# Kernel optimization log

Measured on AMD Instinct MI355X. Metric: run time of the kernel, lower is better.

## Reference

```python
import jax, jax.numpy as jnp
import numpy as np

N = 50000
E = 800000
D = 128
NCLASS = 10


def setup_inputs() -> dict:
    key = jax.random.key(0)
    ks = jax.random.split(key, 12)
    stdv = 1.0 / np.sqrt(D)
    inp = {
        "x": jax.random.normal(ks[0], (N, D), dtype=jnp.float32),
        "edge_src": jax.random.randint(ks[1], (E,), 0, N, dtype=jnp.int32),
        "edge_dst": jax.random.randint(ks[2], (E,), 0, N, dtype=jnp.int32),
        "edge_weight": jax.random.uniform(ks[3], (E,), dtype=jnp.float32),
        "W1": jax.random.uniform(ks[4], (D, D), jnp.float32, -stdv, stdv),
        "b1": jax.random.uniform(ks[5], (D,), jnp.float32, -stdv, stdv),
        "W2": jax.random.uniform(ks[6], (D, D), jnp.float32, -stdv, stdv),
        "b2": jax.random.uniform(ks[7], (D,), jnp.float32, -stdv, stdv),
        "W3": jax.random.uniform(ks[8], (D, D), jnp.float32, -stdv, stdv),
        "b3": jax.random.uniform(ks[9], (D,), jnp.float32, -stdv, stdv),
        "lin_W": jax.random.normal(ks[10], (NCLASS, 3 * D), dtype=jnp.float32) * 0.05,
        "lin_b": jax.random.normal(ks[11], (NCLASS,), dtype=jnp.float32) * 0.05,
    }
    return inp


def _gcn_layer(h, W, b, edge_src, edge_dst, edge_weight):
    # support = h @ W  (dense GEMM), then spmm(adj, support) as gather-scale-scatter
    support = h @ W                                   # [N, out]
    msgs = support[edge_src] * edge_weight[:, None]   # [E, out]
    agg = jax.ops.segment_sum(msgs, edge_dst, num_segments=h.shape[0])
    return agg + b


def reference(x, edge_src, edge_dst, edge_weight, W1, b1, W2, b2, W3, b3, lin_W, lin_b):
    x1 = jax.nn.relu(_gcn_layer(x, W1, b1, edge_src, edge_dst, edge_weight))
    o1 = jnp.max(x1, axis=0)
    x2 = jax.nn.relu(_gcn_layer(x1, W2, b2, edge_src, edge_dst, edge_weight))
    o2 = jnp.max(x2, axis=0)
    x3 = _gcn_layer(x2, W3, b3, edge_src, edge_dst, edge_weight)
    o3 = jnp.max(x3, axis=0)
    lin_in = jnp.concatenate([o1, o2, o3], axis=0)    # [3*D]
    logits = lin_W @ lin_in + lin_b                   # [nclass]
    return jax.nn.log_softmax(logits, axis=0)
```

## Files before the change

kernel.cpp:

```cpp
#include <hip/hip_runtime.h>
#include <hip/hip_bf16.h>
#include <math.h>

#define NN 50000
#define NPAD 50048
#define NE 800000
#define DD 128
#define NCLS 10
#define SCAN_BLOCK 1024
#define NTILES ((NN + 1 + SCAN_BLOCK - 1) / SCAN_BLOCK)

typedef short s16x8 __attribute__((ext_vector_type(8)));
typedef float f32x4 __attribute__((ext_vector_type(4)));

__device__ __forceinline__ unsigned short f2bf(float x) {
  __hip_bfloat16 h = __float2bfloat16(x);
  return __builtin_bit_cast(unsigned short, h);
}
__device__ __forceinline__ float bflo(unsigned int u) { return __uint_as_float(u << 16); }
__device__ __forceinline__ float bfhi(unsigned int u) { return __uint_as_float(u & 0xFFFF0000u); }

__device__ __forceinline__ unsigned int fkey(float f) {
  unsigned int u = __float_as_uint(f);
  return u ^ ((u & 0x80000000u) ? 0xFFFFFFFFu : 0x80000000u);
}
__device__ __forceinline__ float funkey(unsigned int k) {
  unsigned int u = (k & 0x80000000u) ? (k ^ 0x80000000u) : ~k;
  return __uint_as_float(u);
}

__global__ void k_init(int* __restrict__ offs, unsigned int* __restrict__ omax) {
  int i = blockIdx.x * blockDim.x + threadIdx.x;
  if (i < NN + 1) offs[i] = 0;
  if (i < 3 * DD) omax[i] = 0u;
}

__global__ void k_count(const int* __restrict__ edst, int* __restrict__ offs) {
  int e = blockIdx.x * blockDim.x + threadIdx.x;
  if (e < NE) atomicAdd(&offs[edst[e] + 1], 1);
}

__global__ void k_scan_partial(const int* __restrict__ offs, int* __restrict__ bsum) {
  __shared__ int red[SCAN_BLOCK];
  int i = blockIdx.x * SCAN_BLOCK + threadIdx.x;
  red[threadIdx.x] = (i < NN + 1) ? offs[i] : 0;
  __syncthreads();
  for (int off = SCAN_BLOCK / 2; off > 0; off >>= 1) {
    if ((int)threadIdx.x < off) red[threadIdx.x] += red[threadIdx.x + off];
    __syncthreads();
  }
  if (threadIdx.x == 0) bsum[blockIdx.x] = red[0];
}

__global__ void k_scan_bsum(int* __restrict__ bsum) {
  if (threadIdx.x == 0) {
    int run = 0;
    for (int i = 0; i < NTILES; ++i) { int v = bsum[i]; bsum[i] = run; run += v; }
  }
}

__global__ void k_scan_final(int* __restrict__ offs, const int* __restrict__ bsum,
                             int* __restrict__ cursor) {
  __shared__ int tmp[SCAN_BLOCK];
  int i = blockIdx.x * SCAN_BLOCK + threadIdx.x;
  int v = (i < NN + 1) ? offs[i] : 0;
  tmp[threadIdx.x] = v;
  __syncthreads();
  for (int off = 1; off < SCAN_BLOCK; off <<= 1) {
    int t = ((int)threadIdx.x >= off) ? tmp[threadIdx.x - off] : 0;
    __syncthreads();
    tmp[threadIdx.x] += t;
    __syncthreads();
  }
  int incl = tmp[threadIdx.x] + bsum[blockIdx.x];
  if (i < NN + 1) {
    offs[i] = incl;
    if (i < NN) cursor[i] = incl;
  }
}

__global__ void k_fill(const int* __restrict__ esrc, const int* __restrict__ edst,
                       const float* __restrict__ ew, int* __restrict__ cursor,
                       int2* __restrict__ csr) {
  int e = blockIdx.x * blockDim.x + threadIdx.x;
  if (e < NE) {
    int d = edst[e];
    int p = atomicAdd(&cursor[d], 1);
    csr[p] = make_int2(esrc[e], __float_as_int(ew[e]));
  }
}

__global__ __launch_bounds__(256) void k_cvtW(const float* __restrict__ W1,
    const float* __restrict__ W2, const float* __restrict__ W3,
    unsigned short* __restrict__ WT1, unsigned short* __restrict__ WT2,
    unsigned short* __restrict__ WT3) {
  int i = blockIdx.x * 256 + threadIdx.x;
  if (i < DD * DD) {
    int k = i >> 7, c = i & 127;
    WT1[c * DD + k] = f2bf(W1[i]);
    WT2[c * DD + k] = f2bf(W2[i]);
    WT3[c * DD + k] = f2bf(W3[i]);
  }
}

template <int F32IN>
__global__ __launch_bounds__(256) void k_mm(const void* __restrict__ Hv,
                                            const unsigned short* __restrict__ Wt,
                                            unsigned short* __restrict__ S) {
  __shared__ unsigned short Hl[32 * DD];
  char* lb = (char*)Hl;
  const int wave = threadIdx.x >> 6, lane = threadIdx.x & 63;
  const int l15 = lane & 15, lk16 = (lane >> 4);
  const int r0 = blockIdx.x * 32;

#pragma unroll
  for (int j = 0; j < 2; ++j) {
    const int idx = threadIdx.x + j * 256;
    const int B = idx * 16;
    const int row = B >> 8;
    const int addr = B ^ ((row & 7) << 4);
    if (F32IN) {
      const float* H = (const float*)Hv;
      const int r = r0 + row;
      float4 a = make_float4(0.f, 0.f, 0.f, 0.f), b = a;
      if (r < NN) {
        const float* src = H + (size_t)r * DD + ((B & 255) >> 1);
        a = *(const float4*)src;
        b = *(const float4*)(src + 4);
      }
      uint4 pv;
      pv.x = (uint)f2bf(a.x) | ((uint)f2bf(a.y) << 16);
      pv.y = (uint)f2bf(a.z) | ((uint)f2bf(a.w) << 16);
      pv.z = (uint)f2bf(b.x) | ((uint)f2bf(b.y) << 16);
      pv.w = (uint)f2bf(b.z) | ((uint)f2bf(b.w) << 16);
      *(uint4*)(lb + addr) = pv;
    } else {
      const char* H = (const char*)Hv;
      uint4 v = *(const uint4*)(H + (size_t)r0 * 256 + B);
      *(uint4*)(lb + addr) = v;
    }
  }
  __syncthreads();

  const int cbase = wave * 32;
  s16x8 Af[2][4];
#pragma unroll
  for (int m = 0; m < 2; ++m)
#pragma unroll
    for (int ks = 0; ks < 4; ++ks)
      Af[m][ks] = *(const s16x8*)&Wt[(cbase + m * 16 + l15) * DD + ks * 32 + lk16 * 8];

  s16x8 Bf[2][4];
#pragma unroll
  for (int n = 0; n < 2; ++n) {
    const int row = n * 16 + l15;
#pragma unroll
    for (int ks = 0; ks < 4; ++ks) {
      const int B = row * 256 + ks * 64 + lk16 * 16;
      Bf[n][ks] = *(const s16x8*)(lb + (B ^ ((row & 7) << 4)));
    }
  }

  f32x4 acc[2][2];
#pragma unroll
  for (int m = 0; m < 2; ++m)
#pragma unroll
    for (int n = 0; n < 2; ++n) acc[m][n] = (f32x4){0.f, 0.f, 0.f, 0.f};

#pragma unroll
  for (int ks = 0; ks < 4; ++ks)
#pragma unroll
    for (int m = 0; m < 2; ++m)
#pragma unroll
      for (int n = 0; n < 2; ++n)
        acc[m][n] = __builtin_amdgcn_mfma_f32_16x16x32_bf16(Af[m][ks], Bf[n][ks],
                                                            acc[m][n], 0, 0, 0);

  __syncthreads();
#pragma unroll
  for (int m = 0; m < 2; ++m)
#pragma unroll
    for (int n = 0; n < 2; ++n) {
      const int row = n * 16 + l15;
      const int colb = (cbase + m * 16 + 4 * lk16) * 2;
      const int B = row * 256 + colb;
      uint2 pv;
      pv.x = (uint)f2bf(acc[m][n][0]) | ((uint)f2bf(acc[m][n][1]) << 16);
      pv.y = (uint)f2bf(acc[m][n][2]) | ((uint)f2bf(acc[m][n][3]) << 16);
      *(uint2*)(lb + (B ^ ((row & 7) << 4))) = pv;
    }
  __syncthreads();
#pragma unroll
  for (int j = 0; j < 2; ++j) {
    const int idx = threadIdx.x + j * 256;
    const int B = idx * 16;
    const int row = B >> 8;
    uint4 v = *(const uint4*)(lb + (B ^ ((row & 7) << 4)));
    *(uint4*)((char*)S + (size_t)r0 * 256 + B) = v;
  }
}

__device__ __forceinline__ void fma8(float* acc, float w, uint4 u) {
  acc[0] = fmaf(w, bflo(u.x), acc[0]);
  acc[1] = fmaf(w, bfhi(u.x), acc[1]);
  acc[2] = fmaf(w, bflo(u.y), acc[2]);
  acc[3] = fmaf(w, bfhi(u.y), acc[3]);
  acc[4] = fmaf(w, bflo(u.z), acc[4]);
  acc[5] = fmaf(w, bfhi(u.z), acc[5]);
  acc[6] = fmaf(w, bflo(u.w), acc[6]);
  acc[7] = fmaf(w, bfhi(u.w), acc[7]);
}

__global__ __launch_bounds__(256) void k_agg(const unsigned short* __restrict__ S,
                                             const int2* __restrict__ csr,
                                             const int* __restrict__ offs,
                                             const float* __restrict__ bias,
                                             unsigned short* __restrict__ Xout,
                                             unsigned int* __restrict__ omax,
                                             int do_relu) {
  __shared__ unsigned int cmax[DD];
  for (int i = threadIdx.x; i < DD; i += 256) cmax[i] = 0u;
  __syncthreads();
  const int lane = threadIdx.x & 63;
  const int wave = threadIdx.x >> 6;
  const int q = lane >> 4;
  const int t = lane & 15;
  const int gwave = blockIdx.x * 4 + wave;
  const int nwaves = gridDim.x * 4;
  const unsigned short* Scol = S + t * 8;

  float bcol[8];
  {
    float4 b0 = *(const float4*)&bias[t * 8];
    float4 b1 = *(const float4*)&bias[t * 8 + 4];
    bcol[0] = b0.x; bcol[1] = b0.y; bcol[2] = b0.z; bcol[3] = b0.w;
    bcol[4] = b1.x; bcol[5] = b1.y; bcol[6] = b1.z; bcol[7] = b1.w;
  }
  float mx[8];
#pragma unroll
  for (int j = 0; j < 8; ++j) mx[j] = -INFINITY;

  for (int d = gwave; d < NN; d += nwaves) {
    const int e0 = offs[d], e1 = offs[d + 1];
    const int nedge = e1 - e0;
    float acc[8] = {0.f, 0.f, 0.f, 0.f, 0.f, 0.f, 0.f, 0.f};
    int e = e0 + q;
    int done = 0;
    for (; done + 32 <= nedge; done += 32, e += 32) {
      int2 a0 = csr[e];      int2 a1 = csr[e + 4];
      int2 a2 = csr[e + 8];  int2 a3 = csr[e + 12];
      int2 a4 = csr[e + 16]; int2 a5 = csr[e + 20];
      int2 a6 = csr[e + 24]; int2 a7 = csr[e + 28];
      uint4 u0 = *(const uint4*)&Scol[(size_t)a0.x * DD];
      uint4 u1 = *(const uint4*)&Scol[(size_t)a1.x * DD];
      uint4 u2 = *(const uint4*)&Scol[(size_t)a2.x * DD];
      uint4 u3 = *(const uint4*)&Scol[(size_t)a3.x * DD];
      uint4 u4 = *(const uint4*)&Scol[(size_t)a4.x * DD];
      uint4 u5 = *(const uint4*)&Scol[(size_t)a5.x * DD];
      uint4 u6 = *(const uint4*)&Scol[(size_t)a6.x * DD];
      uint4 u7 = *(const uint4*)&Scol[(size_t)a7.x * DD];
      fma8(acc, __int_as_float(a0.y), u0);
      fma8(acc, __int_as_float(a1.y), u1);
      fma8(acc, __int_as_float(a2.y), u2);
      fma8(acc, __int_as_float(a3.y), u3);
      fma8(acc, __int_as_float(a4.y), u4);
      fma8(acc, __int_as_float(a5.y), u5);
      fma8(acc, __int_as_float(a6.y), u6);
      fma8(acc, __int_as_float(a7.y), u7);
    }
    if (done + 16 <= nedge) {
      int2 a0 = csr[e];      int2 a1 = csr[e + 4];
      int2 a2 = csr[e + 8];  int2 a3 = csr[e + 12];
      uint4 u0 = *(const uint4*)&Scol[(size_t)a0.x * DD];
      uint4 u1 = *(const uint4*)&Scol[(size_t)a1.x * DD];
      uint4 u2 = *(const uint4*)&Scol[(size_t)a2.x * DD];
      uint4 u3 = *(const uint4*)&Scol[(size_t)a3.x * DD];
      fma8(acc, __int_as_float(a0.y), u0);
      fma8(acc, __int_as_float(a1.y), u1);
      fma8(acc, __int_as_float(a2.y), u2);
      fma8(acc, __int_as_float(a3.y), u3);
      done += 16; e += 16;
    }
    while (__any(e < e1)) {
      if (e < e1) {
        int2 c = csr[e];
        uint4 u = *(const uint4*)&Scol[(size_t)c.x * DD];
        fma8(acc, __int_as_float(c.y), u);
      }
      e += 4;
    }
#pragma unroll
    for (int j = 0; j < 8; ++j) {
      acc[j] += __shfl_xor(acc[j], 16, 64);
      acc[j] += __shfl_xor(acc[j], 32, 64);
      acc[j] += bcol[j];
      if (do_relu) acc[j] = fmaxf(acc[j], 0.f);
      mx[j] = fmaxf(mx[j], acc[j]);
    }
    if (Xout && q == 0) {
      uint4 xv;
      xv.x = (uint)f2bf(acc[0]) | ((uint)f2bf(acc[1]) << 16);
      xv.y = (uint)f2bf(acc[2]) | ((uint)f2bf(acc[3]) << 16);
      xv.z = (uint)f2bf(acc[4]) | ((uint)f2bf(acc[5]) << 16);
      xv.w = (uint)f2bf(acc[6]) | ((uint)f2bf(acc[7]) << 16);
      *(uint4*)&Xout[(size_t)d * DD + t * 8] = xv;
    }
  }
  if (q == 0) {
#pragma unroll
    for (int j = 0; j < 8; ++j) atomicMax(&cmax[t * 8 + j], fkey(mx[j]));
  }
  __syncthreads();
  for (int i = threadIdx.x; i < DD; i += 256) atomicMax(&omax[i], cmax[i]);
}

__global__ void k_head(const unsigned int* __restrict__ omax,
                       const float* __restrict__ linW,
                       const float* __restrict__ linb,
                       float* __restrict__ out) {
  __shared__ float o[3 * DD];
  __shared__ float logits[NCLS];
  int t = threadIdx.x;
  if (t < 3 * DD) o[t] = funkey(omax[t]);
  __syncthreads();
  if (t < NCLS) {
    float acc = linb[t];
    for (int j = 0; j < 3 * DD; ++j) acc = fmaf(linW[t * 3 * DD + j], o[j], acc);
    logits[t] = acc;
  }
  __syncthreads();
  if (t == 0) {
    float m = -INFINITY;
    for (int c = 0; c < NCLS; ++c) m = fmaxf(m, logits[c]);
    float s = 0.f;
    for (int c = 0; c < NCLS; ++c) s += expf(logits[c] - m);
    float ls = logf(s);
    for (int c = 0; c < NCLS; ++c) out[c] = logits[c] - m - ls;
  }
}

extern "C" void kernel_launch(void* const* d_in, const int* in_sizes, int n_in,
                              void* d_out, int out_size, void* d_ws, size_t ws_size,
                              hipStream_t stream) {
  const float* x    = (const float*)d_in[0];
  const int*   esrc = (const int*)d_in[1];
  const int*   edst = (const int*)d_in[2];
  const float* ew   = (const float*)d_in[3];
  const float* W1   = (const float*)d_in[4];
  const float* b1   = (const float*)d_in[5];
  const float* W2   = (const float*)d_in[6];
  const float* b2   = (const float*)d_in[7];
  const float* W3   = (const float*)d_in[8];
  const float* b3   = (const float*)d_in[9];
  const float* linW = (const float*)d_in[10];
  const float* linb = (const float*)d_in[11];
  float* out = (float*)d_out;

  size_t off = 0;
  auto alloc = [&](size_t bytes) {
    void* p = (char*)d_ws + off;
    off += (bytes + 255) & ~(size_t)255;
    return p;
  };
  unsigned short* X1   = (unsigned short*)alloc((size_t)NPAD * DD * 2);
  unsigned short* X2   = (unsigned short*)alloc((size_t)NPAD * DD * 2);
  unsigned short* S    = (unsigned short*)alloc((size_t)NPAD * DD * 2);
  unsigned short* WT1  = (unsigned short*)alloc((size_t)DD * DD * 2);
  unsigned short* WT2  = (unsigned short*)alloc((size_t)DD * DD * 2);
  unsigned short* WT3  = (unsigned short*)alloc((size_t)DD * DD * 2);
  int*          offs   = (int*)alloc((NN + 1) * 4);
  int*          cursor = (int*)alloc(NN * 4);
  int2*         csr    = (int2*)alloc((size_t)NE * 8);
  unsigned int* omax   = (unsigned int*)alloc(3 * DD * 4);
  int*          bsum   = (int*)alloc(NTILES * 4);
  (void)ws_size; (void)n_in; (void)in_sizes; (void)out_size;

  k_init<<<(NN + 256) / 256, 256, 0, stream>>>(offs, omax);
  k_count<<<(NE + 255) / 256, 256, 0, stream>>>(edst, offs);
  k_scan_partial<<<NTILES, SCAN_BLOCK, 0, stream>>>(offs, bsum);
  k_scan_bsum<<<1, 64, 0, stream>>>(bsum);
  k_scan_final<<<NTILES, SCAN_BLOCK, 0, stream>>>(offs, bsum, cursor);
  k_fill<<<(NE + 255) / 256, 256, 0, stream>>>(esrc, edst, ew, cursor, csr);

  k_cvtW<<<(DD * DD + 255) / 256, 256, 0, stream>>>(W1, W2, W3, WT1, WT2, WT3);

  const int mm_grid = NPAD / 32;
  k_mm<1><<<mm_grid, 256, 0, stream>>>(x, WT1, S);
  k_agg<<<2048, 256, 0, stream>>>(S, csr, offs, b1, X1, omax, 1);
  k_mm<0><<<mm_grid, 256, 0, stream>>>(X1, WT2, S);
  k_agg<<<2048, 256, 0, stream>>>(S, csr, offs, b2, X2, omax + DD, 1);
  k_mm<0><<<mm_grid, 256, 0, stream>>>(X2, WT3, S);
  k_agg<<<2048, 256, 0, stream>>>(S, csr, offs, b3, nullptr, omax + 2 * DD, 0);

  k_head<<<1, 384, 0, stream>>>(omax, linW, linb, out);
}
```

Before: 429.1 us.

## Store GEMM output as custom 8-bit float and decode via shared LUT in aggregation

The dense GEMM now packs its output into a custom 8-bit float (4-bit exponent, 3-bit mantissa, produced by way of fp16 rounding) instead of bf16. This halves the bytes gathered per edge in the memory-bound aggregation kernel. The aggregation decodes each byte through a 256-entry float lookup table in shared memory, and its unroll depth drops from 8 to 4 edges per lane. The init kernel is also replaced by hipMemsetAsync, with the omax zeroing folded into the weight-convert kernel. The main risk is accuracy: 3 mantissa bits and a narrow exponent range flush small values to zero and clamp large ones, and the LUT reads add shared-memory traffic and possible bank conflicts.

```diff
diff --git a/kernel.cpp b/kernel.cpp
--- a/kernel.cpp
+++ b/kernel.cpp
@@ -1,5 +1,6 @@
 #include <hip/hip_runtime.h>
 #include <hip/hip_bf16.h>
+#include <hip/hip_fp16.h>
 #include <math.h>
 
 #define NN 50000
@@ -17,8 +18,21 @@
   __hip_bfloat16 h = __float2bfloat16(x);
   return __builtin_bit_cast(unsigned short, h);
 }
-__device__ __forceinline__ float bflo(unsigned int u) { return __uint_as_float(u << 16); }
-__device__ __forceinline__ float bfhi(unsigned int u) { return __uint_as_float(u & 0xFFFF0000u); }
+
+__device__ __forceinline__ unsigned int f2fp8(float x) {
+  unsigned short h = __builtin_bit_cast(unsigned short, __float2half(x));
+  unsigned int s = (unsigned int)(h >> 15) << 7;
+  int e = (h >> 10) & 31;
+  unsigned int m = h & 1023u;
+  if (e > 23) return s | 0x7E;
+  if (e <= 8) return s;
+  unsigned int add = 0x3F + ((m >> 7) & 1u);
+  m += add;
+  if (m > 1023u) { m = 0; e += 1; if (e > 23) return s | 0x7E; }
+  unsigned int r = s | ((unsigned int)(e - 8) << 3) | (m >> 7);
+  if ((r & 0x7F) == 0x7F) r = s | 0x7E;
+  return r;
+}
 
 __device__ __forceinline__ unsigned int fkey(float f) {
   unsigned int u = __float_as_uint(f);
@@ -27,12 +41,6 @@
 __device__ __forceinline__ float funkey(unsigned int k) {
   unsigned int u = (k & 0x80000000u) ? (k ^ 0x80000000u) : ~k;
   return __uint_as_float(u);
-}
-
-__global__ void k_init(int* __restrict__ offs, unsigned int* __restrict__ omax) {
-  int i = blockIdx.x * blockDim.x + threadIdx.x;
-  if (i < NN + 1) offs[i] = 0;
-  if (i < 3 * DD) omax[i] = 0u;
 }
 
 __global__ void k_count(const int* __restrict__ edst, int* __restrict__ offs) {
@@ -93,8 +101,9 @@
 __global__ __launch_bounds__(256) void k_cvtW(const float* __restrict__ W1,
     const float* __restrict__ W2, const float* __restrict__ W3,
     unsigned short* __restrict__ WT1, unsigned short* __restrict__ WT2,
-    unsigned short* __restrict__ WT3) {
+    unsigned short* __restrict__ WT3, unsigned int* __restrict__ omax) {
   int i = blockIdx.x * 256 + threadIdx.x;
+  if (i < 3 * DD) omax[i] = 0u;
   if (i < DD * DD) {
     int k = i >> 7, c = i & 127;
     WT1[c * DD + k] = f2bf(W1[i]);
@@ -106,7 +115,7 @@
 template <int F32IN>
 __global__ __launch_bounds__(256) void k_mm(const void* __restrict__ Hv,
                                             const unsigned short* __restrict__ Wt,
-                                            unsigned short* __restrict__ S) {
+                                            unsigned char* __restrict__ Sout) {
   __shared__ unsigned short Hl[32 * DD];
   char* lb = (char*)Hl;
   const int wave = threadIdx.x >> 6, lane = threadIdx.x & 63;
@@ -182,43 +191,48 @@
 #pragma unroll
     for (int n = 0; n < 2; ++n) {
       const int row = n * 16 + l15;
-      const int colb = (cbase + m * 16 + 4 * lk16) * 2;
-      const int B = row * 256 + colb;
-      uint2 pv;
-      pv.x = (uint)f2bf(acc[m][n][0]) | ((uint)f2bf(acc[m][n][1]) << 16);
-      pv.y = (uint)f2bf(acc[m][n][2]) | ((uint)f2bf(acc[m][n][3]) << 16);
-      *(uint2*)(lb + (B ^ ((row & 7) << 4))) = pv;
-    }
-  __syncthreads();
-#pragma unroll
-  for (int j = 0; j < 2; ++j) {
-    const int idx = threadIdx.x + j * 256;
-    const int B = idx * 16;
-    const int row = B >> 8;
+      const int colb = cbase + m * 16 + 4 * lk16;
+      const int B = row * 128 + colb;
+      unsigned int pv = f2fp8(acc[m][n][0]) | (f2fp8(acc[m][n][1]) << 8)
+                      | (f2fp8(acc[m][n][2]) << 16) | (f2fp8(acc[m][n][3]) << 24);
+      *(unsigned int*)(lb + (B ^ ((row & 7) << 4))) = pv;
+    }
+  __syncthreads();
+  {
+    const int B = threadIdx.x * 16;
+    const int row = B >> 7;
     uint4 v = *(const uint4*)(lb + (B ^ ((row & 7) << 4)));
-    *(uint4*)((char*)S + (size_t)r0 * 256 + B) = v;
-  }
-}
-
-__device__ __forceinline__ void fma8(float* acc, float w, uint4 u) {
-  acc[0] = fmaf(w, bflo(u.x), acc[0]);
-  acc[1] = fmaf(w, bfhi(u.x), acc[1]);
-  acc[2] = fmaf(w, bflo(u.y), acc[2]);
-  acc[3] = fmaf(w, bfhi(u.y), acc[3]);
-  acc[4] = fmaf(w, bflo(u.z), acc[4]);
-  acc[5] = fmaf(w, bfhi(u.z), acc[5]);
-  acc[6] = fmaf(w, bflo(u.w), acc[6]);
-  acc[7] = fmaf(w, bfhi(u.w), acc[7]);
-}
-
-__global__ __launch_bounds__(256) void k_agg(const unsigned short* __restrict__ S,
+    *(uint4*)(Sout + (size_t)r0 * 128 + B) = v;
+  }
+}
+
+__device__ __forceinline__ void fma8l(float* acc, float w, uint2 u,
+                                      const float* __restrict__ lut) {
+  acc[0] = fmaf(w, lut[u.x & 255u], acc[0]);
+  acc[1] = fmaf(w, lut[(u.x >> 8) & 255u], acc[1]);
+  acc[2] = fmaf(w, lut[(u.x >> 16) & 255u], acc[2]);
+  acc[3] = fmaf(w, lut[u.x >> 24], acc[3]);
+  acc[4] = fmaf(w, lut[u.y & 255u], acc[4]);
+  acc[5] = fmaf(w, lut[(u.y >> 8) & 255u], acc[5]);
+  acc[6] = fmaf(w, lut[(u.y >> 16) & 255u], acc[6]);
+  acc[7] = fmaf(w, lut[u.y >> 24], acc[7]);
+}
+
+__global__ __launch_bounds__(256) void k_agg(const unsigned char* __restrict__ S,
                                              const int2* __restrict__ csr,
                                              const int* __restrict__ offs,
                                              const float* __restrict__ bias,
                                              unsigned short* __restrict__ Xout,
                                              unsigned int* __restrict__ omax,
                                              int do_relu) {
+  __shared__ float lut[256];
   __shared__ unsigned int cmax[DD];
+  {
+    int b = threadIdx.x;
+    int e = (b >> 3) & 15, m = b & 7;
+    float v = e ? ldexpf((float)(8 + m), e - 10) : ldexpf((float)m, -9);
+    lut[b] = (b & 0x80) ? -v : v;
+  }
   for (int i = threadIdx.x; i < DD; i += 256) cmax[i] = 0u;
   __syncthreads();
   const int lane = threadIdx.x & 63;
@@ -227,7 +241,7 @@
   const int t = lane & 15;
   const int gwave = blockIdx.x * 4 + wave;
   const int nwaves = gridDim.x * 4;
-  const unsigned short* Scol = S + t * 8;
+  const unsigned char* Sc = S + t * 8;
 
   float bcol[8];
   {
@@ -246,46 +260,23 @@
     float acc[8] = {0.f, 0.f, 0.f, 0.f, 0.f, 0.f, 0.f, 0.f};
     int e = e0 + q;
     int done = 0;
-    for (; done + 32 <= nedge; done += 32, e += 32) {
+    for (; done + 16 <= nedge; done += 16, e += 16) {
       int2 a0 = csr[e];      int2 a1 = csr[e + 4];
       int2 a2 = csr[e + 8];  int2 a3 = csr[e + 12];
-      int2 a4 = csr[e + 16]; int2 a5 = csr[e + 20];
-      int2 a6 = csr[e + 24]; int2 a7 = csr[e + 28];
-      uint4 u0 = *(const uint4*)&Scol[(size_t)a0.x * DD];
-      uint4 u1 = *(const uint4*)&Scol[(size_t)a1.x * DD];
-      uint4 u2 = *(const uint4*)&Scol[(size_t)a2.x * DD];
-      uint4 u3 = *(const uint4*)&Scol[(size_t)a3.x * DD];
-      uint4 u4 = *(const uint4*)&Scol[(size_t)a4.x * DD];
-      uint4 u5 = *(const uint4*)&Scol[(size_t)a5.x * DD];
-      uint4 u6 = *(const uint4*)&Scol[(size_t)a6.x * DD];
-      uint4 u7 = *(const uint4*)&Scol[(size_t)a7.x * DD];
-      fma8(acc, __int_as_float(a0.y), u0);
-      fma8(acc, __int_as_float(a1.y), u1);
-      fma8(acc, __int_as_float(a2.y), u2);
-      fma8(acc, __int_as_float(a3.y), u3);
-      fma8(acc, __int_as_float(a4.y), u4);
-      fma8(acc, __int_as_float(a5.y), u5);
-      fma8(acc, __int_as_float(a6.y), u6);
-      fma8(acc, __int_as_float(a7.y), u7);
-    }
-    if (done + 16 <= nedge) {
-      int2 a0 = csr[e];      int2 a1 = csr[e + 4];
-      int2 a2 = csr[e + 8];  int2 a3 = csr[e + 12];
-      uint4 u0 = *(const uint4*)&Scol[(size_t)a0.x * DD];
-      uint4 u1 = *(const uint4*)&Scol[(size_t)a1.x * DD];
-      uint4 u2 = *(const uint4*)&Scol[(size_t)a2.x * DD];
-      uint4 u3 = *(const uint4*)&Scol[(size_t)a3.x * DD];
-      fma8(acc, __int_as_float(a0.y), u0);
-      fma8(acc, __int_as_float(a1.y), u1);
-      fma8(acc, __int_as_float(a2.y), u2);
-      fma8(acc, __int_as_float(a3.y), u3);
-      done += 16; e += 16;
+      uint2 u0 = *(const uint2*)&Sc[(size_t)a0.x * DD];
+      uint2 u1 = *(const uint2*)&Sc[(size_t)a1.x * DD];
+      uint2 u2 = *(const uint2*)&Sc[(size_t)a2.x * DD];
+      uint2 u3 = *(const uint2*)&Sc[(size_t)a3.x * DD];
+      fma8l(acc, __int_as_float(a0.y), u0, lut);
+      fma8l(acc, __int_as_float(a1.y), u1, lut);
+      fma8l(acc, __int_as_float(a2.y), u2, lut);
+      fma8l(acc, __int_as_float(a3.y), u3, lut);
     }
     while (__any(e < e1)) {
       if (e < e1) {
         int2 c = csr[e];
-        uint4 u = *(const uint4*)&Scol[(size_t)c.x * DD];
-        fma8(acc, __int_as_float(c.y), u);
+        uint2 u = *(const uint2*)&Sc[(size_t)c.x * DD];
+        fma8l(acc, __int_as_float(c.y), u, lut);
       }
       e += 4;
     }
@@ -364,25 +355,25 @@
   };
   unsigned short* X1   = (unsigned short*)alloc((size_t)NPAD * DD * 2);
   unsigned short* X2   = (unsigned short*)alloc((size_t)NPAD * DD * 2);
-  unsigned short* S    = (unsigned short*)alloc((size_t)NPAD * DD * 2);
+  unsigned char*  S    = (unsigned char*)alloc((size_t)NPAD * DD);
   unsigned short* WT1  = (unsigned short*)alloc((size_t)DD * DD * 2);
   unsigned short* WT2  = (unsigned short*)alloc((size_t)DD * DD * 2);
   unsigned short* WT3  = (unsigned short*)alloc((size_t)DD * DD * 2);
-  int*          offs   = (int*)alloc((NN + 1) * 4);
+  int*          offs   = (int*)alloc((NN + 2) * 4);
   int*          cursor = (int*)alloc(NN * 4);
   int2*         csr    = (int2*)alloc((size_t)NE * 8);
   unsigned int* omax   = (unsigned int*)alloc(3 * DD * 4);
   int*          bsum   = (int*)alloc(NTILES * 4);
   (void)ws_size; (void)n_in; (void)in_sizes; (void)out_size;
 
-  k_init<<<(NN + 256) / 256, 256, 0, stream>>>(offs, omax);
+  hipMemsetAsync(offs, 0, (NN + 2) * 4, stream);
   k_count<<<(NE + 255) / 256, 256, 0, stream>>>(edst, offs);
   k_scan_partial<<<NTILES, SCAN_BLOCK, 0, stream>>>(offs, bsum);
   k_scan_bsum<<<1, 64, 0, stream>>>(bsum);
   k_scan_final<<<NTILES, SCAN_BLOCK, 0, stream>>>(offs, bsum, cursor);
   k_fill<<<(NE + 255) / 256, 256, 0, stream>>>(esrc, edst, ew, cursor, csr);
 
-  k_cvtW<<<(DD * DD + 255) / 256, 256, 0, stream>>>(W1, W2, W3, WT1, WT2, WT3);
+  k_cvtW<<<(DD * DD + 255) / 256, 256, 0, stream>>>(W1, W2, W3, WT1, WT2, WT3, omax);
 
   const int mm_grid = NPAD / 32;
   k_mm<1><<<mm_grid, 256, 0, stream>>>(x, WT1, S);
```

Result: no change. 435.7 us (+1.5%).
